# Performance work log

Measured on AMD Instinct MI355X. Metric: run time of the kernel, lower is better.

## Reference

```python
import jax, jax.numpy as jnp
import numpy as np

V, N, D, C = 3, 4096, 512, 10
PSI = 0.7
CE_SCALE = 0.1


def setup_inputs() -> dict:
    key = jax.random.key(0)
    ks = jax.random.split(key, 10)
    X = jax.random.normal(ks[0], (V, N, D), jnp.float32)
    # sparse-ish symmetric binary adjacency per view (dense storage, as in source)
    A = (jax.random.uniform(ks[1], (V, N, N)) < 0.01).astype(jnp.float32)
    A = jnp.maximum(A, jnp.swapaxes(A, 1, 2))
    # ce_scale * Dirichlet(alpha=ones(C)) samples, one per (view, node)
    consensus = CE_SCALE * jax.random.dirichlet(ks[2], jnp.ones((C,), jnp.float32), (V, N)).astype(jnp.float32)
    W_mlp = jax.random.normal(ks[3], (V, D, C), jnp.float32) * 0.05
    b_mlp = jnp.zeros((V, C), jnp.float32)
    W1 = jax.random.normal(ks[4], (V, D, D), jnp.float32) * 0.05
    b1 = jnp.zeros((V, D), jnp.float32)
    W2 = jax.random.normal(ks[5], (V, D, C), jnp.float32) * 0.05
    b2 = jnp.zeros((V, C), jnp.float32)
    return {"X": X, "A": A, "consensus": consensus, "W_mlp": W_mlp, "b_mlp": b_mlp,
            "W1": W1, "b1": b1, "W2": W2, "b2": b2}


def _gcn_norm(A):
    # A: [V, N, N].  A_hat = A + I;  A_norm = D^{-1/2} A_hat D^{-1/2}
    A_hat = A + jnp.eye(A.shape[-1], dtype=A.dtype)
    dinv = 1.0 / jnp.sqrt(jnp.sum(A_hat, axis=-1))          # [V, N]
    return dinv[:, :, None] * A_hat * dinv[:, None, :]


def reference(X, A, consensus, W_mlp, b_mlp, W1, b1, W2, b2):
    # --- EvidenceCollector (single Linear -> Softplus; dropout is eval-identity) ---
    mlp = jax.nn.softplus(jnp.einsum('vnd,vdc->vnc', X, W_mlp) + b_mlp[:, None, :])
    # --- GCN: softplus(gcn2(gcn1(X, A), A)) ---
    A_norm = _gcn_norm(A)                                    # [V, N, N]
    h = jnp.einsum('vij,vjd->vid', A_norm, X)
    h = jnp.einsum('vnd,vde->vne', h, W1) + b1[:, None, :]   # gcn1 linear
    h = jnp.einsum('vij,vjc->vic', A_norm, h)
    gcn = jax.nn.softplus(jnp.einsum('vnd,vdc->vnc', h, W2) + b2[:, None, :])
    E = consensus + mlp + gcn                                # evidences, [V, N, C]

    # --- create_complete_graph: mean cosine similarity per view-pair (i<j) ---
    En = E / jnp.clip(jnp.linalg.norm(E, axis=-1, keepdims=True), 1e-8)
    S = jnp.einsum('inc,jnc->ij', En, En) / E.shape[1]       # [V, V] mean cos-sim
    mask = jnp.triu(jnp.ones((V, V), bool), k=1)             # edges (i, j), i<j
    max_sim = jnp.max(jnp.where(mask, S, -jnp.inf))
    thr = PSI * max_sim
    w = jnp.where(mask & (S > thr), S, 0.0)                  # thresholded weights

    # --- mrf_aggregate: per-source-row softmax over its edges, weighted sum ---
    logits = jnp.where(mask, w, -1e30)
    m = jnp.max(logits, axis=1, keepdims=True)
    e = jnp.exp(logits - m) * mask                           # zero for non-edges
    p = e / jnp.clip(jnp.sum(e, axis=1, keepdims=True), 1e-30)  # empty rows -> 0
    # sum_{i,j>i} p[i,j] * (E[j] + E[i])
    agg = jnp.einsum('ij,jnc->nc', p, E) + jnp.einsum('i,inc->nc', jnp.sum(p, axis=1), E)
    agg = agg / (2.0 * V)
    return (E, agg)
```

## Files before the change

kernel.cpp:

```cpp
#include <hip/hip_runtime.h>
#include <stdint.h>
#include <stddef.h>

#define VV 3
#define NN 4096
#define DD 512
#define CC 10

typedef unsigned short bf16_t;
typedef __attribute__((ext_vector_type(8))) short bf16x8;
typedef __attribute__((ext_vector_type(4))) float f32x4;

#define MFMA16 __builtin_amdgcn_mfma_f32_16x16x32_bf16

__device__ __forceinline__ float bf2f(unsigned u) {
  union { unsigned u; float f; } c; c.u = u << 16; return c.f;
}
__device__ __forceinline__ bf16_t f2bf(float f) {
  union { float f; unsigned u; } c; c.f = f;
  unsigned r = (c.u + 0x7FFFu + ((c.u >> 16) & 1u)) >> 16;
  return (bf16_t)r;
}
__device__ __forceinline__ float splus(float x) {
  float ax = fabsf(x);
  return fmaxf(x, 0.0f) + log1pf(expf(-ax));
}

__global__ __launch_bounds__(256) void k_prep(const float* __restrict__ A,
    const float* __restrict__ W1, const float* __restrict__ b1,
    const float* __restrict__ W2, const float* __restrict__ W_mlp,
    unsigned long long* __restrict__ mask, float* __restrict__ dinv,
    bf16_t* __restrict__ Wc_t, float* __restrict__ bp, bf16_t* __restrict__ Wm_t)
{
  int t = threadIdx.x;
  if (blockIdx.x < VV * NN / 4) {
    int wid = blockIdx.x * 4 + (t >> 6);
    int lane = t & 63;
    const float* row = A + (size_t)wid * NN;
    unsigned long long myw = 0ull;
#pragma unroll 8
    for (int it = 0; it < 64; ++it) {
      float x = row[it * 64 + lane];
      unsigned long long b = __ballot(x != 0.0f);
      if (lane == it) myw = b;
    }
    mask[(size_t)wid * 64 + lane] = myw;
    int pc = __popcll(myw);
#pragma unroll
    for (int s = 32; s; s >>= 1) pc += __shfl_xor(pc, s);
    if (lane == 0) dinv[wid] = 1.0f / sqrtf((float)(pc + 1));
  } else if (blockIdx.x < VV * NN / 4 + 385) {
    int blk = blockIdx.x - VV * NN / 4;
    int wid = blk * 4 + (t >> 6);
    int lane = t & 63;
    if (wid >= VV * 513) return;
    int v = wid / 513, dd2 = wid % 513;
    const float* w2 = W2 + (size_t)v * DD * CC;
    const float* src = (dd2 < DD) ? (W1 + ((size_t)v * DD + dd2) * DD) : (b1 + (size_t)v * DD);
    float acc[CC];
#pragma unroll
    for (int c = 0; c < CC; ++c) acc[c] = 0.f;
    for (int it = 0; it < 8; ++it) {
      int e = it * 64 + lane;
      float w = src[e];
      const float* w2r = w2 + (size_t)e * CC;
#pragma unroll
      for (int c = 0; c < CC; ++c) acc[c] += w * w2r[c];
    }
#pragma unroll
    for (int c = 0; c < CC; ++c) {
#pragma unroll
      for (int s = 32; s; s >>= 1) acc[c] += __shfl_xor(acc[c], s);
    }
    if (lane == 0) {
      if (dd2 < DD) {
#pragma unroll
        for (int c = 0; c < CC; ++c) Wc_t[((size_t)v * 16 + c) * DD + dd2] = f2bf(acc[c]);
#pragma unroll
        for (int c = CC; c < 16; ++c) Wc_t[((size_t)v * 16 + c) * DD + dd2] = 0;
      } else {
#pragma unroll
        for (int c = 0; c < CC; ++c) bp[v * CC + c] = acc[c];
      }
    }
  } else {
    int idx = (blockIdx.x - (VV * NN / 4 + 385)) * 256 + t;
    if (idx >= VV * DD) return;
    int v = idx / DD, d = idx % DD;
#pragma unroll
    for (int c = 0; c < CC; ++c)
      Wm_t[((size_t)v * 16 + c) * DD + d] = f2bf(W_mlp[((size_t)v * DD + d) * CC + c]);
#pragma unroll
    for (int c = CC; c < 16; ++c) Wm_t[((size_t)v * 16 + c) * DD + d] = 0;
  }
}

__global__ __launch_bounds__(256) void k_zs(
    const float* __restrict__ X,
    const bf16_t* __restrict__ Wc_t, const bf16_t* __restrict__ Wm_t,
    const float* __restrict__ b_mlp, const float* __restrict__ consensus,
    const float* __restrict__ dinv,
    unsigned* __restrict__ Ps1p, float* __restrict__ Epart)
{
  __shared__ bf16_t Bc[16 * 520];
  __shared__ bf16_t Bm[16 * 520];
  int v = blockIdx.y;
  int t = threadIdx.x;
  {
    int r = t & 15, ch = t >> 4;
    const bf16_t* sc = Wc_t + (size_t)v * 16 * DD + (size_t)r * DD + ch * 32;
    const bf16_t* sm = Wm_t + (size_t)v * 16 * DD + (size_t)r * DD + ch * 32;
    bf16_t* dc = &Bc[r * 520 + ch * 32];
    bf16_t* dm = &Bm[r * 520 + ch * 32];
#pragma unroll
    for (int q = 0; q < 4; ++q) {
      *(bf16x8*)(dc + q * 8) = *(const bf16x8*)(sc + q * 8);
      *(bf16x8*)(dm + q * 8) = *(const bf16x8*)(sm + q * 8);
    }
  }
  __syncthreads();
  int w = t >> 6, lane = t & 63;
  int fl = lane & 15, fh = lane >> 4;
  int r0 = blockIdx.x * 64 + w * 16;
  const float* Xrow = X + ((size_t)v * NN + r0 + fl) * DD;
  f32x4 aP = {0.f, 0.f, 0.f, 0.f}, aM = {0.f, 0.f, 0.f, 0.f};
#pragma unroll
  for (int k = 0; k < 16; ++k) {
    float4 x0 = *(const float4*)(Xrow + k * 32 + fh * 8);
    float4 x1 = *(const float4*)(Xrow + k * 32 + fh * 8 + 4);
    bf16x8 a = { (short)f2bf(x0.x), (short)f2bf(x0.y), (short)f2bf(x0.z), (short)f2bf(x0.w),
                 (short)f2bf(x1.x), (short)f2bf(x1.y), (short)f2bf(x1.z), (short)f2bf(x1.w) };
    bf16x8 b1v = *(const bf16x8*)(&Bc[fl * 520 + k * 32 + fh * 8]);
    aP = MFMA16(a, b1v, aP, 0, 0, 0);
    bf16x8 b2v = *(const bf16x8*)(&Bm[fl * 520 + k * 32 + fh * 8]);
    aM = MFMA16(a, b2v, aM, 0, 0, 0);
  }
  float bmv = (fl < CC) ? b_mlp[v * CC + fl] : 0.f;
#pragma unroll
  for (int g = 0; g < 4; ++g) {
    int j = r0 + fh * 4 + g;
    float dj = dinv[v * NN + j];
    float val = aP[g] * dj;
    float part = __shfl_xor(val, 1);
    if (((fl & 1) == 0) && fl < CC) {
      unsigned pw = (unsigned)f2bf(val) | ((unsigned)f2bf(part) << 16);
      Ps1p[((size_t)v * 5 + (fl >> 1)) * NN + j] = pw;
    }
    if (fl < CC) {
      size_t ad = ((size_t)v * NN + j) * CC + fl;
      Epart[ad] = consensus[ad] + splus(aM[g] + bmv);
    }
  }
}

#define SPMM_PROLOG(SRC_) \
  __shared__ unsigned PsL[5 * NN];   \
  int v = blockIdx.y; \
  int t = threadIdx.x; \
  { \
    const uint4* src_ = (const uint4*)((SRC_) + (size_t)v * 5 * NN); \
    uint4* dst_ = (uint4*)PsL; \
    _Pragma("unroll") \
    for (int q = 0; q < 20; ++q) dst_[q * 256 + t] = src_[q * 256 + t]; \
  } \
  __syncthreads(); \
  int w = t >> 6, g = (t >> 3) & 7, s = t & 7; \
  int i = blockIdx.x * 32 + w * 8 + g; \
  const unsigned long long* mrow = mask + ((size_t)v * NN + i) * 64; \
  float acc[CC]; \
  _Pragma("unroll") \
  for (int c = 0; c < CC; ++c) acc[c] = 0.f; \
  _Pragma("unroll") \
  for (int it = 0; it < 8; ++it) { \
    unsigned long long bits = mrow[it * 8 + s]; \
    int jb = (it * 8 + s) * 64; \
    while (bits) { \
      int b = __builtin_ctzll(bits); \
      bits &= bits - 1; \
      int j = jb + b; \
      _Pragma("unroll") \
      for (int c2 = 0; c2 < 5; ++c2) { \
        unsigned pw = PsL[c2 * NN + j]; \
        acc[2 * c2]     += bf2f(pw & 0xFFFFu); \
        acc[2 * c2 + 1] += bf2f(pw >> 16); \
      } \
    } \
  } \
  _Pragma("unroll") \
  for (int c = 0; c < CC; ++c) { \
    acc[c] += __shfl_xor(acc[c], 1); \
    acc[c] += __shfl_xor(acc[c], 2); \
    acc[c] += __shfl_xor(acc[c], 4); \
  }

__global__ __launch_bounds__(256) void k_spmm1(
    const unsigned long long* __restrict__ mask, const unsigned* __restrict__ Ps1p,
    const float* __restrict__ bp, const float* __restrict__ dinv,
    unsigned* __restrict__ P2p)
{
  SPMM_PROLOG(Ps1p)
  if (s == 0) {
    float di = dinv[v * NN + i];
#pragma unroll
    for (int c2 = 0; c2 < 5; ++c2) {
      unsigned pw = PsL[c2 * NN + i];
      acc[2 * c2]     += bf2f(pw & 0xFFFFu);
      acc[2 * c2 + 1] += bf2f(pw >> 16);
    }
#pragma unroll
    for (int c2 = 0; c2 < 5; ++c2) {
      float lo = di * (di * acc[2 * c2]     + bp[v * CC + 2 * c2]);
      float hi = di * (di * acc[2 * c2 + 1] + bp[v * CC + 2 * c2 + 1]);
      P2p[((size_t)v * 5 + c2) * NN + i] = (unsigned)f2bf(lo) | ((unsigned)f2bf(hi) << 16);
    }
  }
}

__global__ __launch_bounds__(256) void k_spmm2(
    const unsigned long long* __restrict__ mask, const unsigned* __restrict__ P2p,
    const float* __restrict__ b2, const float* __restrict__ dinv,
    float* __restrict__ E)
{
  SPMM_PROLOG(P2p)
  if (s == 0) {
    float di = dinv[v * NN + i];
#pragma unroll
    for (int c2 = 0; c2 < 5; ++c2) {
      unsigned pw = PsL[c2 * NN + i];
      acc[2 * c2]     += bf2f(pw & 0xFFFFu);
      acc[2 * c2 + 1] += bf2f(pw >> 16);
    }
    float* Eo = E + ((size_t)v * NN + i) * CC;
#pragma unroll
    for (int c = 0; c < CC; ++c)
      Eo[c] = Eo[c] + splus(di * acc[c] + b2[v * CC + c]);
  }
}

__global__ __launch_bounds__(256) void k_sim(const float* __restrict__ E,
                                             float* __restrict__ partial)
{
  __shared__ float sm[3][256];
  int t = threadIdx.x;
  int n = blockIdx.x * 256 + t;
  float e0[CC], e1[CC], e2[CC];
#pragma unroll
  for (int c = 0; c < CC; ++c) {
    e0[c] = E[(size_t)(0 * NN + n) * CC + c];
    e1[c] = E[(size_t)(1 * NN + n) * CC + c];
    e2[c] = E[(size_t)(2 * NN + n) * CC + c];
  }
  float n0 = 0, n1 = 0, n2 = 0, d01 = 0, d02 = 0, d12 = 0;
#pragma unroll
  for (int c = 0; c < CC; ++c) { n0 += e0[c]*e0[c]; n1 += e1[c]*e1[c]; n2 += e2[c]*e2[c]; }
  float i0 = 1.0f / fmaxf(sqrtf(n0), 1e-8f);
  float i1 = 1.0f / fmaxf(sqrtf(n1), 1e-8f);
  float i2 = 1.0f / fmaxf(sqrtf(n2), 1e-8f);
#pragma unroll
  for (int c = 0; c < CC; ++c) { d01 += e0[c]*e1[c]; d02 += e0[c]*e2[c]; d12 += e1[c]*e2[c]; }
  sm[0][t] = d01 * i0 * i1;
  sm[1][t] = d02 * i0 * i2;
  sm[2][t] = d12 * i1 * i2;
  __syncthreads();
  for (int s = 128; s; s >>= 1) {
    if (t < s) { sm[0][t] += sm[0][t+s]; sm[1][t] += sm[1][t+s]; sm[2][t] += sm[2][t+s]; }
    __syncthreads();
  }
  if (t == 0) {
    partial[blockIdx.x * 3 + 0] = sm[0][0];
    partial[blockIdx.x * 3 + 1] = sm[1][0];
    partial[blockIdx.x * 3 + 2] = sm[2][0];
  }
}

__global__ __launch_bounds__(256) void k_aggc(const float* __restrict__ E,
    const float* __restrict__ partial, float* __restrict__ agg)
{
  float S01 = 0, S02 = 0, S12 = 0;
  for (int b = 0; b < NN / 256; ++b) {
    S01 += partial[b * 3 + 0];
    S02 += partial[b * 3 + 1];
    S12 += partial[b * 3 + 2];
  }
  S01 /= (float)NN; S02 /= (float)NN; S12 /= (float)NN;
  float mx = fmaxf(S01, fmaxf(S02, S12));
  float thr = 0.7f * mx;
  float w01 = (S01 > thr) ? S01 : 0.f;
  float w02 = (S02 > thr) ? S02 : 0.f;
  float m0 = fmaxf(w01, w02);
  float e01 = expf(w01 - m0), e02 = expf(w02 - m0);
  float s0 = e01 + e02;
  float p01 = e01 / s0, p02 = e02 / s0;
  float p12 = 1.0f;
  float c0 = (p01 + p02) / 6.0f;
  float c1 = (p12 + p01) / 6.0f;
  float c2 = (p02 + p12) / 6.0f;
  int idx = blockIdx.x * 256 + threadIdx.x;
  agg[idx] = c0 * E[idx] + c1 * E[NN * CC + idx] + c2 * E[2 * NN * CC + idx];
}

extern "C" void kernel_launch(void* const* d_in, const int* in_sizes, int n_in,
                              void* d_out, int out_size, void* d_ws, size_t ws_size,
                              hipStream_t stream)
{
  (void)in_sizes; (void)n_in; (void)out_size;
  const float* X         = (const float*)d_in[0];
  const float* A         = (const float*)d_in[1];
  const float* consensus = (const float*)d_in[2];
  const float* W_mlp     = (const float*)d_in[3];
  const float* b_mlp     = (const float*)d_in[4];
  const float* W1        = (const float*)d_in[5];
  const float* b1        = (const float*)d_in[6];
  const float* W2        = (const float*)d_in[7];
  const float* b2        = (const float*)d_in[8];
  float* Eout = (float*)d_out;
  float* aggout = Eout + (size_t)VV * NN * CC;

  char* ws = (char*)d_ws;
  size_t off = 0;
  auto alloc = [&](size_t b) { char* p = ws + off; off += (b + 255) & ~(size_t)255; return p; };
  unsigned long long* mask = (unsigned long long*)alloc((size_t)VV * NN * 64 * 8);
  float*  dinv  = (float*) alloc((size_t)VV * NN * 4);
  bf16_t* Wc_t  = (bf16_t*)alloc((size_t)VV * 16 * DD * 2);
  bf16_t* Wm_t  = (bf16_t*)alloc((size_t)VV * 16 * DD * 2);
  float*  bp    = (float*) alloc((size_t)VV * CC * 4);
  unsigned* Ps1p = (unsigned*)alloc((size_t)VV * 5 * NN * 4);
  unsigned* P2p  = (unsigned*)alloc((size_t)VV * 5 * NN * 4);
  float*  partial = (float*)alloc((NN / 256) * 3 * 4);
  if (off > ws_size) return;

  k_prep <<<VV * NN / 4 + 385 + 6, 256, 0, stream>>>(A, W1, b1, W2, W_mlp,
                                                     mask, dinv, Wc_t, bp, Wm_t);
  k_zs   <<<dim3(NN / 64, VV), 256, 0, stream>>>(X, Wc_t, Wm_t, b_mlp, consensus,
                                                 dinv, Ps1p, Eout);
  k_spmm1<<<dim3(NN / 32, VV), 256, 0, stream>>>(mask, Ps1p, bp, dinv, P2p);
  k_spmm2<<<dim3(NN / 32, VV), 256, 0, stream>>>(mask, P2p, b2, dinv, Eout);
  k_sim  <<<NN / 256, 256, 0, stream>>>(Eout, partial);
  k_aggc <<<NN * CC / 256, 256, 0, stream>>>(Eout, partial, aggout);
}
```

Measured before the change: 82.55 us.

## Vectorize adjacency mask build and fuse similarity and aggregation via grid barrier

```diff
diff --git a/kernel.cpp b/kernel.cpp
--- a/kernel.cpp
+++ b/kernel.cpp
@@ -33,26 +33,30 @@
     bf16_t* __restrict__ Wc_t, float* __restrict__ bp, bf16_t* __restrict__ Wm_t)
 {
   int t = threadIdx.x;
+  int w = t >> 6, lane = t & 63;
   if (blockIdx.x < VV * NN / 4) {
-    int wid = blockIdx.x * 4 + (t >> 6);
-    int lane = t & 63;
-    const float* row = A + (size_t)wid * NN;
+    size_t row = (size_t)blockIdx.x * 4 + w;
+    const f32x4* r4 = (const f32x4*)(A + row * NN);
     unsigned long long myw = 0ull;
 #pragma unroll 8
-    for (int it = 0; it < 64; ++it) {
-      float x = row[it * 64 + lane];
-      unsigned long long b = __ballot(x != 0.0f);
-      if (lane == it) myw = b;
-    }
-    mask[(size_t)wid * 64 + lane] = myw;
+    for (int it = 0; it < 16; ++it) {
+      f32x4 x = __builtin_nontemporal_load(r4 + it * 64 + lane);
+      unsigned long long q0 = __ballot(x[0] != 0.0f);
+      unsigned long long q1 = __ballot(x[1] != 0.0f);
+      unsigned long long q2 = __ballot(x[2] != 0.0f);
+      unsigned long long q3 = __ballot(x[3] != 0.0f);
+      if ((lane >> 2) == it) {
+        int k = lane & 3;
+        myw = (k == 0) ? q0 : (k == 1) ? q1 : (k == 2) ? q2 : q3;
+      }
+    }
+    mask[row * 64 + lane] = myw;
     int pc = __popcll(myw);
 #pragma unroll
     for (int s = 32; s; s >>= 1) pc += __shfl_xor(pc, s);
-    if (lane == 0) dinv[wid] = 1.0f / sqrtf((float)(pc + 1));
+    if (lane == 0) dinv[row] = 1.0f / sqrtf((float)(pc + 1));
   } else if (blockIdx.x < VV * NN / 4 + 385) {
-    int blk = blockIdx.x - VV * NN / 4;
-    int wid = blk * 4 + (t >> 6);
-    int lane = t & 63;
+    int wid = (blockIdx.x - VV * NN / 4) * 4 + w;
     if (wid >= VV * 513) return;
     int v = wid / 513, dd2 = wid % 513;
     const float* w2 = W2 + (size_t)v * DD * CC;
@@ -61,11 +65,10 @@
 #pragma unroll
     for (int c = 0; c < CC; ++c) acc[c] = 0.f;
     for (int it = 0; it < 8; ++it) {
-      int e = it * 64 + lane;
-      float w = src[e];
-      const float* w2r = w2 + (size_t)e * CC;
-#pragma unroll
-      for (int c = 0; c < CC; ++c) acc[c] += w * w2r[c];
+      float wv = src[it * 64 + lane];
+      const float* w2r = w2 + (size_t)(it * 64 + lane) * CC;
+#pragma unroll
+      for (int c = 0; c < CC; ++c) acc[c] += wv * w2r[c];
     }
 #pragma unroll
     for (int c = 0; c < CC; ++c) {
@@ -100,7 +103,7 @@
     const bf16_t* __restrict__ Wc_t, const bf16_t* __restrict__ Wm_t,
     const float* __restrict__ b_mlp, const float* __restrict__ consensus,
     const float* __restrict__ dinv,
-    unsigned* __restrict__ Ps1p, float* __restrict__ Epart)
+    unsigned* __restrict__ Ps1p, float* __restrict__ E)
 {
   __shared__ bf16_t Bc[16 * 520];
   __shared__ bf16_t Bm[16 * 520];
@@ -139,7 +142,7 @@
 #pragma unroll
   for (int g = 0; g < 4; ++g) {
     int j = r0 + fh * 4 + g;
-    float dj = dinv[v * NN + j];
+    float dj = dinv[(size_t)v * NN + j];
     float val = aP[g] * dj;
     float part = __shfl_xor(val, 1);
     if (((fl & 1) == 0) && fl < CC) {
@@ -148,7 +151,7 @@
     }
     if (fl < CC) {
       size_t ad = ((size_t)v * NN + j) * CC + fl;
-      Epart[ad] = consensus[ad] + splus(aM[g] + bmv);
+      E[ad] = consensus[ad] + splus(aM[g] + bmv);
     }
   }
 }
@@ -172,12 +175,13 @@
   for (int c = 0; c < CC; ++c) acc[c] = 0.f; \
   _Pragma("unroll") \
   for (int it = 0; it < 8; ++it) { \
-    unsigned long long bits = mrow[it * 8 + s]; \
-    int jb = (it * 8 + s) * 64; \
+    int wi = it * 8 + s; \
+    unsigned long long bits = mrow[wi]; \
+    int jb = (wi >> 2) * 256 + (wi & 3); \
     while (bits) { \
       int b = __builtin_ctzll(bits); \
       bits &= bits - 1; \
-      int j = jb + b; \
+      int j = jb + (b << 2); \
       _Pragma("unroll") \
       for (int c2 = 0; c2 < 5; ++c2) { \
         unsigned pw = PsL[c2 * NN + j]; \
@@ -200,7 +204,7 @@
 {
   SPMM_PROLOG(Ps1p)
   if (s == 0) {
-    float di = dinv[v * NN + i];
+    float di = dinv[(size_t)v * NN + i];
 #pragma unroll
     for (int c2 = 0; c2 < 5; ++c2) {
       unsigned pw = PsL[c2 * NN + i];
@@ -223,7 +227,7 @@
 {
   SPMM_PROLOG(P2p)
   if (s == 0) {
-    float di = dinv[v * NN + i];
+    float di = dinv[(size_t)v * NN + i];
 #pragma unroll
     for (int c2 = 0; c2 < 5; ++c2) {
       unsigned pw = PsL[c2 * NN + i];
@@ -237,47 +241,55 @@
   }
 }
 
-__global__ __launch_bounds__(256) void k_sim(const float* __restrict__ E,
-                                             float* __restrict__ partial)
+__global__ __launch_bounds__(256) void k_tail(const float* __restrict__ E,
+    float* __restrict__ partial, unsigned* __restrict__ barcnt,
+    float* __restrict__ agg)
 {
   __shared__ float sm[3][256];
   int t = threadIdx.x;
-  int n = blockIdx.x * 256 + t;
-  float e0[CC], e1[CC], e2[CC];
-#pragma unroll
-  for (int c = 0; c < CC; ++c) {
-    e0[c] = E[(size_t)(0 * NN + n) * CC + c];
-    e1[c] = E[(size_t)(1 * NN + n) * CC + c];
-    e2[c] = E[(size_t)(2 * NN + n) * CC + c];
-  }
-  float n0 = 0, n1 = 0, n2 = 0, d01 = 0, d02 = 0, d12 = 0;
-#pragma unroll
-  for (int c = 0; c < CC; ++c) { n0 += e0[c]*e0[c]; n1 += e1[c]*e1[c]; n2 += e2[c]*e2[c]; }
-  float i0 = 1.0f / fmaxf(sqrtf(n0), 1e-8f);
-  float i1 = 1.0f / fmaxf(sqrtf(n1), 1e-8f);
-  float i2 = 1.0f / fmaxf(sqrtf(n2), 1e-8f);
-#pragma unroll
-  for (int c = 0; c < CC; ++c) { d01 += e0[c]*e1[c]; d02 += e0[c]*e2[c]; d12 += e1[c]*e2[c]; }
-  sm[0][t] = d01 * i0 * i1;
-  sm[1][t] = d02 * i0 * i2;
-  sm[2][t] = d12 * i1 * i2;
+  int bid = blockIdx.x;
+  if (bid < 16) {
+    int n = bid * 256 + t;
+    float e0[CC], e1[CC], e2[CC];
+#pragma unroll
+    for (int c = 0; c < CC; ++c) {
+      e0[c] = E[(size_t)(0 * NN + n) * CC + c];
+      e1[c] = E[(size_t)(1 * NN + n) * CC + c];
+      e2[c] = E[(size_t)(2 * NN + n) * CC + c];
+    }
+    float n0 = 0, n1 = 0, n2 = 0, d01 = 0, d02 = 0, d12 = 0;
+#pragma unroll
+    for (int c = 0; c < CC; ++c) { n0 += e0[c]*e0[c]; n1 += e1[c]*e1[c]; n2 += e2[c]*e2[c]; }
+    float i0 = 1.0f / fmaxf(sqrtf(n0), 1e-8f);
+    float i1 = 1.0f / fmaxf(sqrtf(n1), 1e-8f);
+    float i2 = 1.0f / fmaxf(sqrtf(n2), 1e-8f);
+#pragma unroll
+    for (int c = 0; c < CC; ++c) { d01 += e0[c]*e1[c]; d02 += e0[c]*e2[c]; d12 += e1[c]*e2[c]; }
+    sm[0][t] = d01 * i0 * i1;
+    sm[1][t] = d02 * i0 * i2;
+    sm[2][t] = d12 * i1 * i2;
+    __syncthreads();
+    for (int s = 128; s; s >>= 1) {
+      if (t < s) { sm[0][t] += sm[0][t+s]; sm[1][t] += sm[1][t+s]; sm[2][t] += sm[2][t+s]; }
+      __syncthreads();
+    }
+    if (t == 0) {
+      partial[bid * 3 + 0] = sm[0][0];
+      partial[bid * 3 + 1] = sm[1][0];
+      partial[bid * 3 + 2] = sm[2][0];
+    }
+  }
   __syncthreads();
-  for (int s = 128; s; s >>= 1) {
-    if (t < s) { sm[0][t] += sm[0][t+s]; sm[1][t] += sm[1][t+s]; sm[2][t] += sm[2][t+s]; }
-    __syncthreads();
-  }
   if (t == 0) {
-    partial[blockIdx.x * 3 + 0] = sm[0][0];
-    partial[blockIdx.x * 3 + 1] = sm[1][0];
-    partial[blockIdx.x * 3 + 2] = sm[2][0];
-  }
-}
-
-__global__ __launch_bounds__(256) void k_aggc(const float* __restrict__ E,
-    const float* __restrict__ partial, float* __restrict__ agg)
-{
+    __builtin_amdgcn_fence(__ATOMIC_RELEASE, "agent");
+    __hip_atomic_fetch_add(barcnt, 1u, __ATOMIC_RELAXED, __HIP_MEMORY_SCOPE_AGENT);
+    while (__hip_atomic_load(barcnt, __ATOMIC_RELAXED, __HIP_MEMORY_SCOPE_AGENT) < 160u)
+      __builtin_amdgcn_s_sleep(8);
+    __builtin_amdgcn_fence(__ATOMIC_ACQUIRE, "agent");
+  }
+  __syncthreads();
   float S01 = 0, S02 = 0, S12 = 0;
-  for (int b = 0; b < NN / 256; ++b) {
+  for (int b = 0; b < 16; ++b) {
     S01 += partial[b * 3 + 0];
     S02 += partial[b * 3 + 1];
     S12 += partial[b * 3 + 2];
@@ -295,7 +307,7 @@
   float c0 = (p01 + p02) / 6.0f;
   float c1 = (p12 + p01) / 6.0f;
   float c2 = (p02 + p12) / 6.0f;
-  int idx = blockIdx.x * 256 + threadIdx.x;
+  int idx = bid * 256 + t;
   agg[idx] = c0 * E[idx] + c1 * E[NN * CC + idx] + c2 * E[2 * NN * CC + idx];
 }
 
@@ -320,21 +332,22 @@
   size_t off = 0;
   auto alloc = [&](size_t b) { char* p = ws + off; off += (b + 255) & ~(size_t)255; return p; };
   unsigned long long* mask = (unsigned long long*)alloc((size_t)VV * NN * 64 * 8);
-  float*  dinv  = (float*) alloc((size_t)VV * NN * 4);
   bf16_t* Wc_t  = (bf16_t*)alloc((size_t)VV * 16 * DD * 2);
   bf16_t* Wm_t  = (bf16_t*)alloc((size_t)VV * 16 * DD * 2);
   float*  bp    = (float*) alloc((size_t)VV * CC * 4);
+  float*  dinv  = (float*) alloc((size_t)VV * NN * 4);
   unsigned* Ps1p = (unsigned*)alloc((size_t)VV * 5 * NN * 4);
   unsigned* P2p  = (unsigned*)alloc((size_t)VV * 5 * NN * 4);
-  float*  partial = (float*)alloc((NN / 256) * 3 * 4);
+  float*  partial = (float*)alloc(16 * 3 * 4);
+  unsigned* barcnt = (unsigned*)alloc(256);
   if (off > ws_size) return;
 
+  hipMemsetAsync(barcnt, 0, 4, stream);
   k_prep <<<VV * NN / 4 + 385 + 6, 256, 0, stream>>>(A, W1, b1, W2, W_mlp,
                                                      mask, dinv, Wc_t, bp, Wm_t);
   k_zs   <<<dim3(NN / 64, VV), 256, 0, stream>>>(X, Wc_t, Wm_t, b_mlp, consensus,
                                                  dinv, Ps1p, Eout);
   k_spmm1<<<dim3(NN / 32, VV), 256, 0, stream>>>(mask, Ps1p, bp, dinv, P2p);
   k_spmm2<<<dim3(NN / 32, VV), 256, 0, stream>>>(mask, P2p, b2, dinv, Eout);
-  k_sim  <<<NN / 256, 256, 0, stream>>>(Eout, partial);
-  k_aggc <<<NN * CC / 256, 256, 0, stream>>>(Eout, partial, aggout);
-}
+  k_tail <<<160, 256, 0, stream>>>(Eout, partial, barcnt, aggout);
+}
```

Result: slower. 97.15 us (+17.7%).
